# Kernel optimization log

Hardware: AMD Instinct MI355X
Metric: run time of the kernel (lower is better)

## Reference

```python
import jax, jax.numpy as jnp
import numpy as np

TGT, SRC, BH, D = 2048, 2048, 16, 64

def setup_inputs() -> dict:
    key = jax.random.key(0)
    kq, kk, kv, km = jax.random.split(key, 4)
    return {
        "query": jax.random.normal(kq, (TGT, BH, D), dtype=jnp.float32),
        "key": jax.random.normal(kk, (SRC, BH, D), dtype=jnp.float32),
        "value": jax.random.normal(kv, (SRC, BH, D), dtype=jnp.float32),
        "attn_mask": jax.random.randint(km, (1, TGT, SRC), 0, 2).astype(jnp.bool_),
    }

def reference(query, key, value, attn_mask):
    # seq-first layout: [len, batch_heads, head_dim] -> [bh, len, d]
    head_dim = query.shape[-1]
    q = jnp.swapaxes(query, 0, 1) * (float(head_dim) ** -0.5)  # [bh, tgt, d]
    k = jnp.swapaxes(key, 0, 1)                                # [bh, src, d]
    v = jnp.swapaxes(value, 0, 1)                              # [bh, src, d]
    w = jnp.einsum('btd,bsd->bts', q, k)                       # [bh, tgt, src]
    w = jnp.where(attn_mask, jnp.float32(-1e8), w)
    w = jax.nn.softmax(w, axis=-1)
    # dropout p=0.0 (eval) -> identity
    out = jnp.einsum('bts,bsd->btd', w, v)                     # [bh, tgt, d]
    return jnp.swapaxes(out, 0, 1), w  # ([tgt, bh, d], [bh, tgt, src])
```

## Files before the change

### kernel.cpp

```cpp
#include <hip/hip_runtime.h>

#define TGT 2048
#define SRC 2048
#define BH 16
#define HD 64
#define BT 16
#define SROW 2056

typedef __bf16 bf16x8 __attribute__((ext_vector_type(8)));
typedef unsigned short ushortx8 __attribute__((ext_vector_type(8)));
typedef float floatx4 __attribute__((ext_vector_type(4)));

__device__ int g_mask_is_u8;

__device__ __forceinline__ unsigned short f2bf(float f) {
  unsigned u = __builtin_bit_cast(unsigned, f);
  u += 0x7FFFu + ((u >> 16) & 1u);
  return (unsigned short)(u >> 16);
}
__device__ __forceinline__ float bf2f(unsigned short s) {
  unsigned u = ((unsigned)s) << 16;
  return __builtin_bit_cast(float, u);
}

__global__ void detect_mask_fmt(const unsigned char* __restrict__ m) {
  __shared__ int any;
  if (threadIdx.x == 0) any = 0;
  __syncthreads();
  int local = 0;
  int base = threadIdx.x * 16;
#pragma unroll
  for (int i = 0; i < 16; ++i) {
    int idx = base + i;
    if (idx & 3) local |= m[idx];
  }
  if (local) atomicOr(&any, 1);
  __syncthreads();
  if (threadIdx.x == 0) g_mask_is_u8 = (any != 0);
}

__global__ void cvt_qk(const float* __restrict__ q, const float* __restrict__ k,
                       unsigned short* __restrict__ qb, unsigned short* __restrict__ kb) {
  const int gid = blockIdx.x * 256 + threadIdx.x;
  const int half = TGT * BH * HD / 8;
  const float* src; unsigned short* dst; float sc;
  int idx;
  if (gid < half) { src = q; dst = qb; sc = 0.125f; idx = gid; }
  else            { src = k; dst = kb; sc = 1.0f;  idx = gid - half; }
  const float* p = src + (size_t)idx * 8;
  float4 a = *(const float4*)p;
  float4 b = *(const float4*)(p + 4);
  union { unsigned short u[8]; ushortx8 v; } o;
  o.u[0] = f2bf(a.x * sc); o.u[1] = f2bf(a.y * sc);
  o.u[2] = f2bf(a.z * sc); o.u[3] = f2bf(a.w * sc);
  o.u[4] = f2bf(b.x * sc); o.u[5] = f2bf(b.y * sc);
  o.u[6] = f2bf(b.z * sc); o.u[7] = f2bf(b.w * sc);
  *(ushortx8*)(dst + (size_t)idx * 8) = o.v;
}

__global__ void v_tr(const float* __restrict__ v, unsigned short* __restrict__ vt) {
  __shared__ unsigned short tile[64 * 72];
  const int h = blockIdx.x >> 5;
  const int s0 = (blockIdx.x & 31) * 64;
  const int tid = threadIdx.x;
  const int sr = tid >> 4, c = tid & 15;
#pragma unroll
  for (int p = 0; p < 4; ++p) {
    const int s = sr + p * 16;
    float4 f = *(const float4*)(v + (size_t)(s0 + s) * (BH * HD) + h * HD + c * 4);
    tile[(c * 4 + 0) * 72 + s] = f2bf(f.x);
    tile[(c * 4 + 1) * 72 + s] = f2bf(f.y);
    tile[(c * 4 + 2) * 72 + s] = f2bf(f.z);
    tile[(c * 4 + 3) * 72 + s] = f2bf(f.w);
  }
  __syncthreads();
  const int d = tid >> 2, q4 = tid & 3;
  ushortx8 o0 = *(const ushortx8*)&tile[d * 72 + q4 * 16];
  ushortx8 o1 = *(const ushortx8*)&tile[d * 72 + q4 * 16 + 8];
  unsigned short* dst = vt + (size_t)h * HD * SRC + (size_t)d * SRC + s0 + q4 * 16;
  *(ushortx8*)dst = o0;
  *(ushortx8*)(dst + 8) = o1;
}

__launch_bounds__(512, 2)
__global__ void attn_kernel(const unsigned short* __restrict__ qb,
                            const unsigned short* __restrict__ kb,
                            const unsigned short* __restrict__ vtb,
                            const unsigned char* __restrict__ mask8,
                            const int* __restrict__ mask32,
                            float* __restrict__ out0,
                            float* __restrict__ wout) {
  extern __shared__ char smem[];
  unsigned short* smS = (unsigned short*)smem;
  float* redArr = (float*)(smem + BT * SROW * 2);
  float* rowmaxArr = redArr + 1024;
  float* invArr = rowmaxArr + BT;

  const int bid0 = blockIdx.x;
  const int bid = (bid0 & 7) * 256 + (bid0 >> 3);
  const int h = bid >> 7;
  const int t0 = (bid & 127) * BT;
  const int tid = threadIdx.x;
  const int wv = tid >> 6;
  const int lane = tid & 63;
  const int quad = lane >> 4;
  const int l16 = lane & 15;
  const bool is_u8 = (g_mask_is_u8 != 0);

  bf16x8 aq[2];
  {
    const unsigned short* qp = qb + (size_t)(t0 + l16) * (BH * HD) + h * HD + quad * 8;
    aq[0] = __builtin_bit_cast(bf16x8, *(const ushortx8*)qp);
    aq[1] = __builtin_bit_cast(bf16x8, *(const ushortx8*)(qp + 32));
  }

  for (int st = wv; st < SRC / 16; st += 8) {
    const int sbase = st * 16;
    const unsigned short* kp = kb + (size_t)(sbase + l16) * (BH * HD) + h * HD + quad * 8;
    bf16x8 bk0 = __builtin_bit_cast(bf16x8, *(const ushortx8*)kp);
    bf16x8 bk1 = __builtin_bit_cast(bf16x8, *(const ushortx8*)(kp + 32));
    floatx4 c = {0.f, 0.f, 0.f, 0.f};
    c = __builtin_amdgcn_mfma_f32_16x16x32_bf16(aq[0], bk0, c, 0, 0, 0);
    c = __builtin_amdgcn_mfma_f32_16x16x32_bf16(aq[1], bk1, c, 0, 0, 0);
    const int scol = sbase + l16;
#pragma unroll
    for (int r = 0; r < 4; ++r) {
      const int tl = quad * 4 + r;
      const float val = c[r];
      const float oth = __shfl_xor(val, 1);
      if (!(l16 & 1)) {
        unsigned pk2 = (unsigned)f2bf(val) | ((unsigned)f2bf(oth) << 16);
        *(unsigned*)&smS[tl * SROW + scol] = pk2;
      }
    }
  }
  __syncthreads();

  {
    const int row = tid >> 5;
    const int cc = tid & 31;
    unsigned short* srow = smS + row * SROW;
    const size_t mbase = (size_t)(t0 + row) * SRC;
    float pmax = -3.4e38f;
#pragma unroll
    for (int kk = 0; kk < 8; ++kk) {
      const int col = cc * 8 + kk * 256;
      ushortx8 u = *(const ushortx8*)&srow[col];
      unsigned mbits[8];
      if (is_u8) {
        uint2 m2 = *(const uint2*)(mask8 + mbase + col);
#pragma unroll
        for (int i = 0; i < 4; ++i) { mbits[i] = (m2.x >> (8 * i)) & 0xFF; mbits[4 + i] = (m2.y >> (8 * i)) & 0xFF; }
      } else {
        const int4 a = *(const int4*)(mask32 + mbase + col);
        const int4 b = *(const int4*)(mask32 + mbase + col + 4);
        mbits[0] = a.x; mbits[1] = a.y; mbits[2] = a.z; mbits[3] = a.w;
        mbits[4] = b.x; mbits[5] = b.y; mbits[6] = b.z; mbits[7] = b.w;
      }
      union { unsigned short u[8]; ushortx8 v; } o;
#pragma unroll
      for (int i = 0; i < 8; ++i) {
        float val = mbits[i] ? -1e8f : bf2f(u[i]);
        pmax = fmaxf(pmax, val);
        o.u[i] = f2bf(val);
      }
      *(ushortx8*)&srow[col] = o.v;
    }
    redArr[row * 32 + cc] = pmax;
  }
  __syncthreads();
  if (tid < BT) {
    float m = -3.4e38f;
    for (int j = 0; j < 32; ++j) m = fmaxf(m, redArr[tid * 32 + j]);
    rowmaxArr[tid] = m;
  }
  __syncthreads();

  {
    const int row = tid >> 5;
    const int cc = tid & 31;
    const float rm = rowmaxArr[row];
    unsigned short* srow = smS + row * SROW;
    float psum = 0.f;
#pragma unroll
    for (int kk = 0; kk < 8; ++kk) {
      const int col = cc * 8 + kk * 256;
      ushortx8 u = *(const ushortx8*)&srow[col];
      union { unsigned short u[8]; ushortx8 v; } o;
#pragma unroll
      for (int i = 0; i < 8; ++i) {
        float e = __expf(bf2f(u[i]) - rm);
        psum += e;
        o.u[i] = f2bf(e);
      }
      *(ushortx8*)&srow[col] = o.v;
    }
    redArr[row * 32 + cc] = psum;
  }
  __syncthreads();
  if (tid < BT) {
    float s = 0.f;
    for (int j = 0; j < 32; ++j) s += redArr[tid * 32 + j];
    invArr[tid] = 1.0f / s;
  }
  __syncthreads();

  {
    const int row = tid >> 5;
    const int cc = tid & 31;
    const float invv = invArr[row];
    float* wrow = wout + ((size_t)h * TGT + (t0 + row)) * SRC;
    const unsigned short* srow = smS + row * SROW;
#pragma unroll
    for (int kk = 0; kk < 8; ++kk) {
      const int col = cc * 8 + kk * 256;
      ushortx8 u = *(const ushortx8*)&srow[col];
      float4 a, b;
      a.x = bf2f(u[0]) * invv; a.y = bf2f(u[1]) * invv;
      a.z = bf2f(u[2]) * invv; a.w = bf2f(u[3]) * invv;
      b.x = bf2f(u[4]) * invv; b.y = bf2f(u[5]) * invv;
      b.z = bf2f(u[6]) * invv; b.w = bf2f(u[7]) * invv;
      *(float4*)&wrow[col] = a;
      *(float4*)&wrow[col + 4] = b;
    }
  }

  {
    const int dt = wv & 3;
    const int halfsel = wv >> 2;
    const int dbase = dt * 16;
    const int sstart = halfsel * 1024;
    const unsigned short* vp = vtb + (size_t)h * HD * SRC +
                               (size_t)(dbase + l16) * SRC + sstart + quad * 8;
    const unsigned short* sp = smS + l16 * SROW + sstart + quad * 8;
    floatx4 acc = {0.f, 0.f, 0.f, 0.f};
    for (int s0 = 0; s0 < 1024; s0 += 32) {
      bf16x8 af = __builtin_bit_cast(bf16x8, *(const ushortx8*)(sp + s0));
      bf16x8 bfv = __builtin_bit_cast(bf16x8, *(const ushortx8*)(vp + s0));
      acc = __builtin_amdgcn_mfma_f32_16x16x32_bf16(af, bfv, acc, 0, 0, 0);
    }
    if (halfsel) {
#pragma unroll
      for (int r = 0; r < 4; ++r)
        redArr[dt * 256 + (quad * 4 + r) * 16 + l16] = acc[r];
    }
    __syncthreads();
    if (!halfsel) {
#pragma unroll
      for (int r = 0; r < 4; ++r) {
        const int tl = quad * 4 + r;
        float s = acc[r] + redArr[dt * 256 + tl * 16 + l16];
        out0[((size_t)(t0 + tl) * BH + h) * HD + dbase + l16] = s * invArr[tl];
      }
    }
  }
}

extern "C" void kernel_launch(void* const* d_in, const int* in_sizes, int n_in,
                              void* d_out, int out_size, void* d_ws, size_t ws_size,
                              hipStream_t stream) {
  const float* q = (const float*)d_in[0];
  const float* k = (const float*)d_in[1];
  const float* v = (const float*)d_in[2];
  const unsigned char* m8 = (const unsigned char*)d_in[3];
  const int* m32 = (const int*)d_in[3];
  float* out0 = (float*)d_out;
  float* wout = out0 + (size_t)TGT * BH * HD;

  unsigned short* qb = (unsigned short*)d_ws;
  unsigned short* kb = qb + (size_t)TGT * BH * HD;
  unsigned short* vt = kb + (size_t)SRC * BH * HD;

  const size_t shbytes = (size_t)BT * SROW * 2 + 1024 * 4 + BT * 4 + BT * 4;
  hipFuncSetAttribute((const void*)attn_kernel,
                      hipFuncAttributeMaxDynamicSharedMemorySize, (int)shbytes);

  detect_mask_fmt<<<1, 256, 0, stream>>>(m8);
  cvt_qk<<<dim3(2048), dim3(256), 0, stream>>>(q, k, qb, kb);
  v_tr<<<dim3(BH * (SRC / 64)), dim3(256), 0, stream>>>(v, vt);
  attn_kernel<<<dim3(BH * (TGT / BT)), dim3(512), shbytes, stream>>>(
      qb, kb, vt, m8, m32, out0, wout);
}
```

Baseline: 442.7 us.

## Pack mask into bitmask, fuse masking and row-max into QK stage, use 1024 threads

Adds a pre-pass that packs the boolean mask into one bit per element, so each attention block reads 4 KB of mask instead of re-reading the full byte or int mask for every one of the 16 heads. Masking and the partial row-max are now applied right after the QK MFMA, which removes one full shared-memory pass over the score tile. Blocks grow to 1024 threads, and the PV reduction is split four ways. This costs an extra kernel launch, more shared memory, and a launch bound of (1024, 8) that may not match what the hardware can actually fit.

```diff
diff --git a/kernel.cpp b/kernel.cpp
--- a/kernel.cpp
+++ b/kernel.cpp
@@ -37,6 +37,35 @@
   if (local) atomicOr(&any, 1);
   __syncthreads();
   if (threadIdx.x == 0) g_mask_is_u8 = (any != 0);
+}
+
+__global__ void mask_pack(const unsigned char* __restrict__ m8,
+                          const int* __restrict__ m32,
+                          unsigned char* __restrict__ bm) {
+  const int gid = blockIdx.x * 256 + threadIdx.x;
+  const bool is_u8 = (g_mask_is_u8 != 0);
+  const size_t base = (size_t)gid * 32;
+  unsigned bits = 0;
+  if (is_u8) {
+    const uint4 a = *(const uint4*)(m8 + base);
+    const uint4 b = *(const uint4*)(m8 + base + 16);
+    unsigned w[8] = {a.x, a.y, a.z, a.w, b.x, b.y, b.z, b.w};
+#pragma unroll
+    for (int wi = 0; wi < 8; ++wi)
+#pragma unroll
+      for (int j = 0; j < 4; ++j)
+        if ((w[wi] >> (8 * j)) & 0xFFu) bits |= 1u << (wi * 4 + j);
+  } else {
+#pragma unroll
+    for (int c = 0; c < 8; ++c) {
+      const int4 a = *(const int4*)(m32 + base + c * 4);
+      if (a.x) bits |= 1u << (c * 4 + 0);
+      if (a.y) bits |= 1u << (c * 4 + 1);
+      if (a.z) bits |= 1u << (c * 4 + 2);
+      if (a.w) bits |= 1u << (c * 4 + 3);
+    }
+  }
+  *(unsigned*)(bm + (size_t)gid * 4) = bits;
 }
 
 __global__ void cvt_qk(const float* __restrict__ q, const float* __restrict__ k,
@@ -82,18 +111,18 @@
   *(ushortx8*)(dst + 8) = o1;
 }
 
-__launch_bounds__(512, 2)
+__launch_bounds__(1024, 8)
 __global__ void attn_kernel(const unsigned short* __restrict__ qb,
                             const unsigned short* __restrict__ kb,
                             const unsigned short* __restrict__ vtb,
-                            const unsigned char* __restrict__ mask8,
-                            const int* __restrict__ mask32,
+                            const unsigned char* __restrict__ bmask,
                             float* __restrict__ out0,
                             float* __restrict__ wout) {
   extern __shared__ char smem[];
   unsigned short* smS = (unsigned short*)smem;
-  float* redArr = (float*)(smem + BT * SROW * 2);
-  float* rowmaxArr = redArr + 1024;
+  float* scratch = (float*)(smem + BT * SROW * 2);
+  float* maxpart = scratch + 3072;
+  float* rowmaxArr = maxpart + 256;
   float* invArr = rowmaxArr + BT;
 
   const int bid0 = blockIdx.x;
@@ -105,7 +134,11 @@
   const int lane = tid & 63;
   const int quad = lane >> 4;
   const int l16 = lane & 15;
-  const bool is_u8 = (g_mask_is_u8 != 0);
+
+  {
+    const unsigned* bg = (const unsigned*)(bmask + (size_t)t0 * (SRC / 8));
+    ((unsigned*)scratch)[tid] = bg[tid];
+  }
 
   bf16x8 aq[2];
   {
@@ -113,8 +146,11 @@
     aq[0] = __builtin_bit_cast(bf16x8, *(const ushortx8*)qp);
     aq[1] = __builtin_bit_cast(bf16x8, *(const ushortx8*)(qp + 32));
   }
-
-  for (int st = wv; st < SRC / 16; st += 8) {
+  __syncthreads();
+
+  const unsigned short* smBits = (const unsigned short*)scratch;
+  float pmax[4] = {-3.4e38f, -3.4e38f, -3.4e38f, -3.4e38f};
+  for (int st = wv; st < SRC / 16; st += 16) {
     const int sbase = st * 16;
     const unsigned short* kp = kb + (size_t)(sbase + l16) * (BH * HD) + h * HD + quad * 8;
     bf16x8 bk0 = __builtin_bit_cast(bf16x8, *(const ushortx8*)kp);
@@ -126,7 +162,9 @@
 #pragma unroll
     for (int r = 0; r < 4; ++r) {
       const int tl = quad * 4 + r;
-      const float val = c[r];
+      const unsigned bits = smBits[tl * (SRC / 16) + st];
+      const float val = ((bits >> l16) & 1u) ? -1e8f : c[r];
+      pmax[r] = fmaxf(pmax[r], val);
       const float oth = __shfl_xor(val, 1);
       if (!(l16 & 1)) {
         unsigned pk2 = (unsigned)f2bf(val) | ((unsigned)f2bf(oth) << 16);
@@ -134,57 +172,32 @@
       }
     }
   }
-  __syncthreads();
-
-  {
-    const int row = tid >> 5;
-    const int cc = tid & 31;
-    unsigned short* srow = smS + row * SROW;
-    const size_t mbase = (size_t)(t0 + row) * SRC;
-    float pmax = -3.4e38f;
-#pragma unroll
-    for (int kk = 0; kk < 8; ++kk) {
-      const int col = cc * 8 + kk * 256;
-      ushortx8 u = *(const ushortx8*)&srow[col];
-      unsigned mbits[8];
-      if (is_u8) {
-        uint2 m2 = *(const uint2*)(mask8 + mbase + col);
-#pragma unroll
-        for (int i = 0; i < 4; ++i) { mbits[i] = (m2.x >> (8 * i)) & 0xFF; mbits[4 + i] = (m2.y >> (8 * i)) & 0xFF; }
-      } else {
-        const int4 a = *(const int4*)(mask32 + mbase + col);
-        const int4 b = *(const int4*)(mask32 + mbase + col + 4);
-        mbits[0] = a.x; mbits[1] = a.y; mbits[2] = a.z; mbits[3] = a.w;
-        mbits[4] = b.x; mbits[5] = b.y; mbits[6] = b.z; mbits[7] = b.w;
-      }
-      union { unsigned short u[8]; ushortx8 v; } o;
-#pragma unroll
-      for (int i = 0; i < 8; ++i) {
-        float val = mbits[i] ? -1e8f : bf2f(u[i]);
-        pmax = fmaxf(pmax, val);
-        o.u[i] = f2bf(val);
-      }
-      *(ushortx8*)&srow[col] = o.v;
-    }
-    redArr[row * 32 + cc] = pmax;
+#pragma unroll
+  for (int r = 0; r < 4; ++r) {
+    float m = pmax[r];
+    m = fmaxf(m, __shfl_xor(m, 1));
+    m = fmaxf(m, __shfl_xor(m, 2));
+    m = fmaxf(m, __shfl_xor(m, 4));
+    m = fmaxf(m, __shfl_xor(m, 8));
+    if (l16 == 0) maxpart[(quad * 4 + r) * 16 + wv] = m;
   }
   __syncthreads();
   if (tid < BT) {
-    float m = -3.4e38f;
-    for (int j = 0; j < 32; ++j) m = fmaxf(m, redArr[tid * 32 + j]);
+    float m = maxpart[tid * 16];
+    for (int j = 1; j < 16; ++j) m = fmaxf(m, maxpart[tid * 16 + j]);
     rowmaxArr[tid] = m;
   }
   __syncthreads();
 
   {
-    const int row = tid >> 5;
-    const int cc = tid & 31;
+    const int row = tid >> 6;
+    const int cc = tid & 63;
     const float rm = rowmaxArr[row];
     unsigned short* srow = smS + row * SROW;
     float psum = 0.f;
 #pragma unroll
-    for (int kk = 0; kk < 8; ++kk) {
-      const int col = cc * 8 + kk * 256;
+    for (int kk = 0; kk < 4; ++kk) {
+      const int col = cc * 8 + kk * 512;
       ushortx8 u = *(const ushortx8*)&srow[col];
       union { unsigned short u[8]; ushortx8 v; } o;
 #pragma unroll
@@ -195,25 +208,25 @@
       }
       *(ushortx8*)&srow[col] = o.v;
     }
-    redArr[row * 32 + cc] = psum;
+    scratch[row * 64 + cc] = psum;
   }
   __syncthreads();
   if (tid < BT) {
     float s = 0.f;
-    for (int j = 0; j < 32; ++j) s += redArr[tid * 32 + j];
+    for (int j = 0; j < 64; ++j) s += scratch[tid * 64 + j];
     invArr[tid] = 1.0f / s;
   }
   __syncthreads();
 
   {
-    const int row = tid >> 5;
-    const int cc = tid & 31;
+    const int row = tid >> 6;
+    const int cc = tid & 63;
     const float invv = invArr[row];
     float* wrow = wout + ((size_t)h * TGT + (t0 + row)) * SRC;
     const unsigned short* srow = smS + row * SROW;
 #pragma unroll
-    for (int kk = 0; kk < 8; ++kk) {
-      const int col = cc * 8 + kk * 256;
+    for (int kk = 0; kk < 4; ++kk) {
+      const int col = cc * 8 + kk * 512;
       ushortx8 u = *(const ushortx8*)&srow[col];
       float4 a, b;
       a.x = bf2f(u[0]) * invv; a.y = bf2f(u[1]) * invv;
@@ -227,29 +240,31 @@
 
   {
     const int dt = wv & 3;
-    const int halfsel = wv >> 2;
+    const int qr = wv >> 2;
     const int dbase = dt * 16;
-    const int sstart = halfsel * 1024;
+    const int sstart = qr * 512;
     const unsigned short* vp = vtb + (size_t)h * HD * SRC +
                                (size_t)(dbase + l16) * SRC + sstart + quad * 8;
     const unsigned short* sp = smS + l16 * SROW + sstart + quad * 8;
     floatx4 acc = {0.f, 0.f, 0.f, 0.f};
-    for (int s0 = 0; s0 < 1024; s0 += 32) {
+    for (int s0 = 0; s0 < 512; s0 += 32) {
       bf16x8 af = __builtin_bit_cast(bf16x8, *(const ushortx8*)(sp + s0));
       bf16x8 bfv = __builtin_bit_cast(bf16x8, *(const ushortx8*)(vp + s0));
       acc = __builtin_amdgcn_mfma_f32_16x16x32_bf16(af, bfv, acc, 0, 0, 0);
     }
-    if (halfsel) {
+    if (qr) {
 #pragma unroll
       for (int r = 0; r < 4; ++r)
-        redArr[dt * 256 + (quad * 4 + r) * 16 + l16] = acc[r];
+        scratch[((qr - 1) * 4 + dt) * 256 + (quad * 4 + r) * 16 + l16] = acc[r];
     }
     __syncthreads();
-    if (!halfsel) {
+    if (!qr) {
 #pragma unroll
       for (int r = 0; r < 4; ++r) {
         const int tl = quad * 4 + r;
-        float s = acc[r] + redArr[dt * 256 + tl * 16 + l16];
+        float s = acc[r] + scratch[(0 * 4 + dt) * 256 + tl * 16 + l16]
+                         + scratch[(1 * 4 + dt) * 256 + tl * 16 + l16]
+                         + scratch[(2 * 4 + dt) * 256 + tl * 16 + l16];
         out0[((size_t)(t0 + tl) * BH + h) * HD + dbase + l16] = s * invArr[tl];
       }
     }
@@ -270,14 +285,16 @@
   unsigned short* qb = (unsigned short*)d_ws;
   unsigned short* kb = qb + (size_t)TGT * BH * HD;
   unsigned short* vt = kb + (size_t)SRC * BH * HD;
-
-  const size_t shbytes = (size_t)BT * SROW * 2 + 1024 * 4 + BT * 4 + BT * 4;
+  unsigned char* bmask = (unsigned char*)(vt + (size_t)BH * HD * SRC);
+
+  const size_t shbytes = (size_t)BT * SROW * 2 + 3072 * 4 + 256 * 4 + BT * 4 + BT * 4;
   hipFuncSetAttribute((const void*)attn_kernel,
                       hipFuncAttributeMaxDynamicSharedMemorySize, (int)shbytes);
 
   detect_mask_fmt<<<1, 256, 0, stream>>>(m8);
+  mask_pack<<<dim3(512), dim3(256), 0, stream>>>(m8, m32, bmask);
   cvt_qk<<<dim3(2048), dim3(256), 0, stream>>>(q, k, qb, kb);
   v_tr<<<dim3(BH * (SRC / 64)), dim3(256), 0, stream>>>(v, vt);
-  attn_kernel<<<dim3(BH * (TGT / BT)), dim3(512), shbytes, stream>>>(
-      qb, kb, vt, m8, m32, out0, wout);
-}
+  attn_kernel<<<dim3(BH * (TGT / BT)), dim3(1024), shbytes, stream>>>(
+      qb, kb, vt, bmask, out0, wout);
+}
```

Result: faster. 433.3 us (-2.1%).
